# Optimization experiments

Hardware: AMD Instinct MI355X
Metric: run time of the kernel (lower is better)

## Reference

```python
import jax, jax.numpy as jnp
import numpy as np

COMMITMENT_COST = 0.25


def setup_inputs() -> dict:
    key = jax.random.key(0)
    k1, k2 = jax.random.split(key)
    inputs = jax.random.normal(k1, (32, 1024, 256), dtype=jnp.float32)
    codebook = jax.random.normal(k2, (8192, 256), dtype=jnp.float32)
    return {"inputs": inputs, "codebook": codebook}


def reference(inputs, codebook):
    input_shape = inputs.shape
    D = codebook.shape[1]
    K = codebook.shape[0]
    flat = inputs.reshape(-1, D)                      # [N, D]
    N = flat.shape[0]

    distances = (
        jnp.sum(flat * flat, axis=1, keepdims=True)
        + jnp.sum(codebook * codebook, axis=1)
        - 2.0 * flat @ codebook.T
    )                                                  # [N, K]
    idx = jnp.argmin(distances, axis=1)               # [N]

    # gather (equivalent to one-hot @ codebook)
    quantized = jnp.take(codebook, idx, axis=0).reshape(input_shape)

    # straight-through estimator
    quantized_st = inputs + jax.lax.stop_gradient(quantized - inputs)

    e_latent_loss = jnp.mean((jax.lax.stop_gradient(quantized_st) - inputs) ** 2)
    q_latent_loss = jnp.mean((quantized - jax.lax.stop_gradient(inputs)) ** 2)
    commitment_loss = COMMITMENT_COST * e_latent_loss
    codebook_loss = q_latent_loss
    vq_loss = commitment_loss + codebook_loss

    # perplexity of codebook usage (avg one-hot probs)
    counts = jnp.zeros((K,), dtype=inputs.dtype).at[idx].add(1.0)
    avg_probs = counts / N
    perplexity = jnp.exp(-jnp.sum(avg_probs * jnp.log(avg_probs + 1e-10)))

    tokens = idx.reshape(input_shape[:-1])
    return quantized_st, tokens, vq_loss, commitment_loss, codebook_loss, perplexity
```

## Files before the change

### kernel.cpp

```cpp
#include <hip/hip_runtime.h>
#include <stdint.h>

typedef unsigned short u16;
typedef unsigned long long u64;

#define N_ROWS 32768
#define DIM 256
#define K_CODES 8192
#define TAU 0.3f

#define A_OFF     0ull
#define B_OFF     16777216ull
#define CN_OFF    20971520ull
#define PART1_OFF 21004288ull
#define PART2_OFF 22052864ull
#define IDX_OFF   22577152ull
#define HIST_OFF  22708224ull
#define CNT_OFF   22740992ull
#define FLAG_OFF  22741008ull
#define LOSS_OFF  22872080ull
#define CBT_OFF   23068672ull
#define GMIN2_OFF 31457280ull

#define OUT_Q 0
#define OUT_T 8388608
#define OUT_S 8421376

#define BM 128
#define BN 128
#define BK 64
#define JSPLIT 4
#define NT (4 * ((K_CODES / JSPLIT) / BN))
#define RSPLIT 4

#define PACK_INF ((((u64)0xFF800000u) << 32) | 0xFFFFFFFFull)

typedef _Float16 half8 __attribute__((ext_vector_type(8)));
typedef float floatx4 __attribute__((ext_vector_type(4)));

__device__ __forceinline__ void gload_lds16(const void* g, void* l) {
    __builtin_amdgcn_global_load_lds(
        (const __attribute__((address_space(1))) void*)g,
        (__attribute__((address_space(3))) void*)l,
        16, 0, 0);
}

__device__ __forceinline__ unsigned sortable(float v) {
    unsigned u = __float_as_uint(v);
    return (u & 0x80000000u) ? ~u : (u | 0x80000000u);
}
__device__ __forceinline__ float unsortable(unsigned u) {
    return (u & 0x80000000u) ? __uint_as_float(u & 0x7fffffffu) : __uint_as_float(~u);
}
__device__ __forceinline__ u64 shfl64x(u64 v, int m) {
    return ((u64)(unsigned)__shfl_xor((int)(v >> 32), m, 64) << 32) |
           (unsigned)__shfl_xor((int)(v & 0xffffffffu), m, 64);
}
__device__ __forceinline__ u64 u64min(u64 a, u64 b) { return a < b ? a : b; }
__device__ __forceinline__ u64 u64max(u64 a, u64 b) { return a > b ? a : b; }

__global__ void prep(const float* __restrict__ inp, const float* __restrict__ cb,
                     u16* __restrict__ A, u16* __restrict__ B, float* __restrict__ cn,
                     unsigned int* __restrict__ hist, int* __restrict__ cnt) {
    if (blockIdx.x >= 5120) {
        int i = (blockIdx.x - 5120) * 256 + threadIdx.x;
        if (i < K_CODES) hist[i] = 0u;
        else if (i < K_CODES + 4) cnt[i - K_CODES] = 0;
        return;
    }
    int g = blockIdx.x * 256 + threadIdx.x;
    int row = g >> 5;
    int kc = (g & 31) << 3;
    bool isA = row < N_ROWS;
    const float* src = isA ? inp + (size_t)row * DIM + kc
                           : cb + (size_t)(row - N_ROWS) * DIM + kc;
    u16* dst = isA ? A + (size_t)row * DIM + kc
                   : B + (size_t)(row - N_ROWS) * DIM + kc;
    float4 x0 = *(const float4*)(src);
    float4 x1 = *(const float4*)(src + 4);
    float xs[8] = {x0.x, x0.y, x0.z, x0.w, x1.x, x1.y, x1.z, x1.w};
    half8 hv;
    float s = 0.f;
#pragma unroll
    for (int i = 0; i < 8; ++i) {
        hv[i] = (_Float16)xs[i];
        s = fmaf(xs[i], xs[i], s);
    }
    *(half8*)(dst) = hv;
    if (!isA) {
#pragma unroll
        for (int m = 1; m <= 16; m <<= 1) s += __shfl_xor(s, m, 64);
        if ((g & 31) == 0) cn[row - N_ROWS] = s;
    }
}

__global__ void transpose_cb(const float* __restrict__ cb, float* __restrict__ cbT) {
    __shared__ float tile[64][65];
    const int tid = threadIdx.x;
    const int tj = blockIdx.x * 64;
    const int td = blockIdx.y * 64;
    const int c = (tid & 15) * 4;
    const int r0 = tid >> 4;
#pragma unroll
    for (int p = 0; p < 4; ++p) {
        int r = p * 16 + r0;
        float4 v = *(const float4*)(cb + (size_t)(tj + r) * DIM + td + c);
        tile[r][c] = v.x; tile[r][c + 1] = v.y; tile[r][c + 2] = v.z; tile[r][c + 3] = v.w;
    }
    __syncthreads();
#pragma unroll
    for (int p = 0; p < 4; ++p) {
        int rr = p * 16 + r0;
        float4 w = {tile[c][rr], tile[c + 1][rr], tile[c + 2][rr], tile[c + 3][rr]};
        *(float4*)(cbT + (size_t)(td + rr) * K_CODES + tj + c) = w;
    }
}

#define STAGE_T(T, BUFI)                                                      \
    {                                                                         \
        const int jc_ = (T) >> 2;                                             \
        const int kk_ = ((T) & 3) * BK;                                       \
        const int colBase_ = jBase + jc_ * BN;                                \
        _Pragma("unroll")                                                     \
        for (int it_ = 0; it_ < 4; ++it_) {                                   \
            int r_ = it_ * 32 + str;                                          \
            int cdat_ = sk16 ^ (r_ & 7);                                      \
            int ch_ = it_ * 256 + tid;                                        \
            gload_lds16(A + (size_t)(rowBase + r_) * DIM + kk_ + cdat_ * 8,   \
                        (char*)lsA[BUFI] + ch_ * 16);                         \
            gload_lds16(B + (size_t)(colBase_ + r_) * DIM + kk_ + cdat_ * 8,  \
                        (char*)lsB[BUFI] + ch_ * 16);                         \
        }                                                                     \
    }

__launch_bounds__(256, 2)
__global__ void vq_pass1(const u16* __restrict__ A, const u16* __restrict__ B,
                         const float* __restrict__ cn,
                         u64* __restrict__ part1, float* __restrict__ part2) {
    __shared__ __align__(16) _Float16 lsA[2][BM * BK];
    __shared__ __align__(16) _Float16 lsB[2][BN * BK];
    __shared__ u64 t1buf[BM];
    __shared__ float t2buf[BM];

    const int tid = threadIdx.x;
    const int lane = tid & 63;
    const int w = tid >> 6;
    const int wm = w >> 1, wn = w & 1;
    const int l15 = lane & 15;
    const int quad = lane >> 4;
    const int xm = l15 & 7;
    const int rowBase = blockIdx.x * BM;
    const int jBase = blockIdx.y * (K_CODES / JSPLIT);

    float d1[16], d2[16];
    unsigned idxr[16];
#pragma unroll
    for (int i = 0; i < 16; ++i) {
        d1[i] = __builtin_inff(); d2[i] = __builtin_inff(); idxr[i] = 0xffffffffu;
    }

    const int str = tid >> 3;
    const int sk16 = tid & 7;

    STAGE_T(0, 0);
    asm volatile("s_waitcnt vmcnt(0)" ::: "memory");
    __builtin_amdgcn_s_barrier();
    asm volatile("" ::: "memory");

    floatx4 acc[4][4];
    int buf = 0;

#pragma unroll 1
    for (int t = 0; t < NT; ++t) {
        if (t + 1 < NT) STAGE_T(t + 1, buf ^ 1);

        if ((t & 3) == 0) {
#pragma unroll
            for (int mi = 0; mi < 4; ++mi)
#pragma unroll
                for (int ni = 0; ni < 4; ++ni)
                    acc[mi][ni] = (floatx4){0.f, 0.f, 0.f, 0.f};
        }

#pragma unroll
        for (int s = 0; s < 2; ++s) {
            const int koff = ((s * 4 + quad) ^ xm) * 8;
            half8 af[4], bf[4];
#pragma unroll
            for (int mi = 0; mi < 4; ++mi)
                af[mi] = *(const half8*)(lsA[buf] + (wm * 64 + mi * 16 + l15) * BK + koff);
#pragma unroll
            for (int ni = 0; ni < 4; ++ni)
                bf[ni] = *(const half8*)(lsB[buf] + (wn * 64 + ni * 16 + l15) * BK + koff);
#pragma unroll
            for (int mi = 0; mi < 4; ++mi)
#pragma unroll
                for (int ni = 0; ni < 4; ++ni)
                    acc[mi][ni] = __builtin_amdgcn_mfma_f32_16x16x32_f16(
                        af[mi], bf[ni], acc[mi][ni], 0, 0, 0);
        }

        if ((t & 3) == 3) {
            const int colBase = jBase + (t >> 2) * BN;
#pragma unroll
            for (int ni = 0; ni < 4; ++ni) {
                unsigned j = (unsigned)(colBase + wn * 64 + ni * 16 + l15);
                float cnj = cn[j];
#pragma unroll
                for (int mi = 0; mi < 4; ++mi) {
#pragma unroll
                    for (int r = 0; r < 4; ++r) {
                        int tr = mi * 4 + r;
                        float val = fmaf(-2.0f, acc[mi][ni][r], cnj);
                        bool lt = val < d1[tr];
                        float sec = lt ? d1[tr] : val;
                        d2[tr] = fminf(d2[tr], sec);
                        d1[tr] = lt ? val : d1[tr];
                        idxr[tr] = lt ? j : idxr[tr];
                    }
                }
            }
        }

        asm volatile("s_waitcnt vmcnt(0)" ::: "memory");
        __builtin_amdgcn_s_barrier();
        asm volatile("" ::: "memory");
        buf ^= 1;
    }

    u64 m1[16];
#pragma unroll
    for (int tr = 0; tr < 16; ++tr)
        m1[tr] = ((u64)sortable(d1[tr]) << 32) | idxr[tr];
#pragma unroll
    for (int m = 1; m <= 8; m <<= 1)
#pragma unroll
        for (int tr = 0; tr < 16; ++tr) {
            u64 o1 = shfl64x(m1[tr], m);
            float o2 = __shfl_xor(d2[tr], m, 64);
            u64 n1 = u64min(m1[tr], o1);
            float big = unsortable((unsigned)(u64max(m1[tr], o1) >> 32));
            d2[tr] = fminf(big, fminf(d2[tr], o2));
            m1[tr] = n1;
        }

    if (wn == 0 && l15 == 0) {
#pragma unroll
        for (int tr = 0; tr < 16; ++tr) {
            int rl = wm * 64 + (tr >> 2) * 16 + quad * 4 + (tr & 3);
            t1buf[rl] = m1[tr]; t2buf[rl] = d2[tr];
        }
    }
    __syncthreads();
    if (wn == 1 && l15 == 0) {
#pragma unroll
        for (int tr = 0; tr < 16; ++tr) {
            int rl = wm * 64 + (tr >> 2) * 16 + quad * 4 + (tr & 3);
            u64 o1 = t1buf[rl];
            float o2 = t2buf[rl];
            u64 n1 = u64min(m1[tr], o1);
            float big = unsortable((unsigned)(u64max(m1[tr], o1) >> 32));
            float n2 = fminf(big, fminf(d2[tr], o2));
            size_t p = (size_t)(rowBase + rl) * JSPLIT + blockIdx.y;
            part1[p] = n1;
            part2[p] = n2;
        }
    }
}

__global__ void vq_merge(const u64* __restrict__ part1, const float* __restrict__ part2,
                         unsigned* __restrict__ idx32,
                         int* __restrict__ flaglist, int* __restrict__ cnt,
                         u64* __restrict__ gmin2) {
    int row = blockIdx.x * 256 + threadIdx.x;
    u64 m1 = PACK_INF;
    float f2 = __builtin_inff();
#pragma unroll
    for (int y = 0; y < JSPLIT; ++y) {
        u64 p1 = part1[(size_t)row * JSPLIT + y];
        float p2 = part2[(size_t)row * JSPLIT + y];
        u64 n1 = u64min(m1, p1);
        float big = unsortable((unsigned)(u64max(m1, p1) >> 32));
        f2 = fminf(big, fminf(f2, p2));
        m1 = n1;
    }
    gmin2[row] = PACK_INF;
    idx32[row] = (unsigned)(m1 & 0xffffffffu);
    float f1 = unsortable((unsigned)(m1 >> 32));
    if (f2 - f1 < TAU) {
        int p = atomicAdd(cnt, 1);
        flaglist[p] = row;
    }
}

__global__ void vq_recompute(const float* __restrict__ inp, const float* __restrict__ cbT,
                             const float* __restrict__ cn, const int* __restrict__ flaglist,
                             const int* __restrict__ cnt, u64* __restrict__ gmin2) {
    __shared__ float xsT[DIM][8];
    __shared__ u64 wred[8][8];
    const int tid = threadIdx.x;
    const int w = tid >> 6, lane = tid & 63;
    const int n = *cnt;
    const int base = blockIdx.x * 8;
    if (base >= n) return;

    {
        int li = base + w;
        int row = flaglist[li < n ? li : (n - 1)];
        float4 a = ((const float4*)(inp + (size_t)row * DIM))[lane];
        int d0 = lane * 4;
        xsT[d0 + 0][w] = a.x; xsT[d0 + 1][w] = a.y;
        xsT[d0 + 2][w] = a.z; xsT[d0 + 3][w] = a.w;
    }
    __syncthreads();

    const int cbase = blockIdx.y * (K_CODES / RSPLIT) + tid * 4;
    float4 acc[8];
#pragma unroll
    for (int r = 0; r < 8; ++r) acc[r] = (float4){0.f, 0.f, 0.f, 0.f};

    float4 cv = *(const float4*)(cbT + cbase);
#pragma unroll 4
    for (int d = 0; d < DIM - 1; ++d) {
        float4 nx = *(const float4*)(cbT + (size_t)(d + 1) * K_CODES + cbase);
        float4 xa = *(const float4*)&xsT[d][0];
        float4 xb = *(const float4*)&xsT[d][4];
        float xv[8] = {xa.x, xa.y, xa.z, xa.w, xb.x, xb.y, xb.z, xb.w};
#pragma unroll
        for (int r = 0; r < 8; ++r) {
            acc[r].x = fmaf(xv[r], cv.x, acc[r].x);
            acc[r].y = fmaf(xv[r], cv.y, acc[r].y);
            acc[r].z = fmaf(xv[r], cv.z, acc[r].z);
            acc[r].w = fmaf(xv[r], cv.w, acc[r].w);
        }
        cv = nx;
    }
    {
        const int d = DIM - 1;
        float4 xa = *(const float4*)&xsT[d][0];
        float4 xb = *(const float4*)&xsT[d][4];
        float xv[8] = {xa.x, xa.y, xa.z, xa.w, xb.x, xb.y, xb.z, xb.w};
#pragma unroll
        for (int r = 0; r < 8; ++r) {
            acc[r].x = fmaf(xv[r], cv.x, acc[r].x);
            acc[r].y = fmaf(xv[r], cv.y, acc[r].y);
            acc[r].z = fmaf(xv[r], cv.z, acc[r].z);
            acc[r].w = fmaf(xv[r], cv.w, acc[r].w);
        }
    }

    u64 best[8];
    float4 cn4 = *(const float4*)(cn + cbase);
#pragma unroll
    for (int r = 0; r < 8; ++r) {
        float d0 = cn4.x - 2.0f * acc[r].x;
        float d1 = cn4.y - 2.0f * acc[r].y;
        float d2 = cn4.z - 2.0f * acc[r].z;
        float d3 = cn4.w - 2.0f * acc[r].w;
        u64 b = ((u64)sortable(d0) << 32) | (unsigned)(cbase + 0);
        b = u64min(b, ((u64)sortable(d1) << 32) | (unsigned)(cbase + 1));
        b = u64min(b, ((u64)sortable(d2) << 32) | (unsigned)(cbase + 2));
        b = u64min(b, ((u64)sortable(d3) << 32) | (unsigned)(cbase + 3));
        best[r] = b;
    }

#pragma unroll
    for (int m = 1; m <= 32; m <<= 1)
#pragma unroll
        for (int r = 0; r < 8; ++r) best[r] = u64min(best[r], shfl64x(best[r], m));
    if (lane < 8) wred[w][lane] = best[lane];
    __syncthreads();
    if (tid < 8 && base + tid < n) {
        u64 b = wred[0][tid];
#pragma unroll
        for (int ww = 1; ww < 8; ++ww) b = u64min(b, wred[ww][tid]);
        atomicMin(&gmin2[flaglist[base + tid]], b);
    }
}

__global__ void vq_writeback(const u64* __restrict__ gmin2, const int* __restrict__ flaglist,
                             const int* __restrict__ cnt, unsigned* __restrict__ idx32) {
    int i = blockIdx.x * 256 + threadIdx.x;
    if (i < *cnt) {
        int row = flaglist[i];
        idx32[row] = (unsigned)(gmin2[row] & 0xffffffffull);
    }
}

__global__ void vq_gather(const float* __restrict__ inp, const float* __restrict__ cb,
                          const unsigned* __restrict__ idx32, float* __restrict__ out,
                          float* __restrict__ losspart, unsigned int* __restrict__ hist) {
    __shared__ float red[4];
    int w = threadIdx.x >> 6, lane = threadIdx.x & 63;
    int i = blockIdx.x * 4 + w;
    unsigned idx = idx32[i];
    float4 c = ((const float4*)(cb + (size_t)idx * DIM))[lane];
    float4 x = ((const float4*)(inp + (size_t)i * DIM))[lane];
    ((float4*)(out + OUT_Q))[(size_t)i * 64 + lane] = c;
    float dx = c.x - x.x, dy = c.y - x.y, dz = c.z - x.z, dw = c.w - x.w;
    float s = dx * dx + dy * dy + dz * dz + dw * dw;
#pragma unroll
    for (int m = 32; m; m >>= 1) s += __shfl_xor(s, m, 64);
    if (lane == 0) {
        out[OUT_T + i] = (float)idx;
        red[w] = s;
        atomicAdd(&hist[idx], 1u);
    }
    __syncthreads();
    if (threadIdx.x == 0)
        losspart[blockIdx.x] = red[0] + red[1] + red[2] + red[3];
}

__global__ void vq_finalize(const unsigned int* __restrict__ hist,
                            const float* __restrict__ losspart, float* __restrict__ out) {
    __shared__ float redp[256], redl[256];
    int tid = threadIdx.x;
    float sp = 0.f, sl = 0.f;
    for (int k = tid; k < K_CODES; k += 256) {
        float p = (float)hist[k] * (1.0f / (float)N_ROWS);
        sp += p * logf(p + 1e-10f);
        sl += losspart[k];
    }
    redp[tid] = sp; redl[tid] = sl;
    __syncthreads();
    for (int st = 128; st; st >>= 1) {
        if (tid < st) { redp[tid] += redp[tid + st]; redl[tid] += redl[tid + st]; }
        __syncthreads();
    }
    if (tid == 0) {
        float perp = expf(-redp[0]);
        float e = redl[0] / 8388608.0f;
        out[OUT_S + 0] = 1.25f * e;
        out[OUT_S + 1] = 0.25f * e;
        out[OUT_S + 2] = e;
        out[OUT_S + 3] = perp;
    }
}

extern "C" void kernel_launch(void* const* d_in, const int* in_sizes, int n_in,
                              void* d_out, int out_size, void* d_ws, size_t ws_size,
                              hipStream_t stream) {
    const float* inp = (const float*)d_in[0];
    const float* cb = (const float*)d_in[1];
    float* out = (float*)d_out;
    char* ws = (char*)d_ws;
    u16* A = (u16*)(ws + A_OFF);
    u16* B = (u16*)(ws + B_OFF);
    float* cn = (float*)(ws + CN_OFF);
    u64* part1 = (u64*)(ws + PART1_OFF);
    float* part2 = (float*)(ws + PART2_OFF);
    unsigned* idx32 = (unsigned*)(ws + IDX_OFF);
    unsigned int* hist = (unsigned int*)(ws + HIST_OFF);
    int* cnt = (int*)(ws + CNT_OFF);
    int* flaglist = (int*)(ws + FLAG_OFF);
    float* losspart = (float*)(ws + LOSS_OFF);
    float* cbT = (float*)(ws + CBT_OFF);
    u64* gmin2 = (u64*)(ws + GMIN2_OFF);

    prep<<<5153, 256, 0, stream>>>(inp, cb, A, B, cn, hist, cnt);
    transpose_cb<<<dim3(K_CODES / 64, DIM / 64), 256, 0, stream>>>(cb, cbT);
    vq_pass1<<<dim3(N_ROWS / BM, JSPLIT), 256, 0, stream>>>(A, B, cn, part1, part2);
    vq_merge<<<N_ROWS / 256, 256, 0, stream>>>(part1, part2, idx32, flaglist, cnt, gmin2);
    vq_recompute<<<dim3(N_ROWS / 8, RSPLIT), 512, 0, stream>>>(inp, cbT, cn, flaglist, cnt, gmin2);
    vq_writeback<<<N_ROWS / 256, 256, 0, stream>>>(gmin2, flaglist, cnt, idx32);
    vq_gather<<<N_ROWS / 4, 256, 0, stream>>>(inp, cb, idx32, out, losspart, hist);
    vq_finalize<<<1, 256, 0, stream>>>(hist, losspart, out);
}
```

Before: 391.6 us.

## Fuse transpose into prep, drop writeback, split top-2 epilogue, persistent recompute grid

Folds the codebook transpose into the prep kernel and removes the separate writeback kernel, so vq_gather now reads gmin2 directly and overrides the index when a recomputed minimum exists. In pass1, JSPLIT drops from 4 to 2, and half of each tile's top-2 distance update is deferred into the next tile's iteration so it can overlap the next stage's loads. The top-2 update now uses fmed3 for the second-best value. vq_recompute becomes a grid-stride loop over a fixed 512-block grid instead of one block per 8 rows. These changes cut kernel launches and idle blocks, at the cost of lower pass1 grid parallelism and gmin2 reads for every row.

```diff
diff --git a/kernel.cpp b/kernel.cpp
--- a/kernel.cpp
+++ b/kernel.cpp
@@ -29,9 +29,10 @@
 #define BM 128
 #define BN 128
 #define BK 64
-#define JSPLIT 4
+#define JSPLIT 2
 #define NT (4 * ((K_CODES / JSPLIT) / BN))
 #define RSPLIT 4
+#define RGRID 512
 
 #define PACK_INF ((((u64)0xFF800000u) << 32) | 0xFFFFFFFFull)
 
@@ -61,14 +62,39 @@
 
 __global__ void prep(const float* __restrict__ inp, const float* __restrict__ cb,
                      u16* __restrict__ A, u16* __restrict__ B, float* __restrict__ cn,
-                     unsigned int* __restrict__ hist, int* __restrict__ cnt) {
+                     unsigned int* __restrict__ hist, int* __restrict__ cnt,
+                     float* __restrict__ cbT) {
+    __shared__ float tile[64][65];
+    const int tid = threadIdx.x;
+
+    if (blockIdx.x >= 5153) {
+        const int bx = blockIdx.x - 5153;
+        const int tj = (bx & 127) * 64;
+        const int td = (bx >> 7) * 64;
+        const int c = (tid & 15) * 4;
+        const int r0 = tid >> 4;
+#pragma unroll
+        for (int p = 0; p < 4; ++p) {
+            int r = p * 16 + r0;
+            float4 v = *(const float4*)(cb + (size_t)(tj + r) * DIM + td + c);
+            tile[r][c] = v.x; tile[r][c + 1] = v.y; tile[r][c + 2] = v.z; tile[r][c + 3] = v.w;
+        }
+        __syncthreads();
+#pragma unroll
+        for (int p = 0; p < 4; ++p) {
+            int rr = p * 16 + r0;
+            float4 w = {tile[c][rr], tile[c + 1][rr], tile[c + 2][rr], tile[c + 3][rr]};
+            *(float4*)(cbT + (size_t)(td + rr) * K_CODES + tj + c) = w;
+        }
+        return;
+    }
     if (blockIdx.x >= 5120) {
-        int i = (blockIdx.x - 5120) * 256 + threadIdx.x;
+        int i = (blockIdx.x - 5120) * 256 + tid;
         if (i < K_CODES) hist[i] = 0u;
         else if (i < K_CODES + 4) cnt[i - K_CODES] = 0;
         return;
     }
-    int g = blockIdx.x * 256 + threadIdx.x;
+    int g = blockIdx.x * 256 + tid;
     int row = g >> 5;
     int kc = (g & 31) << 3;
     bool isA = row < N_ROWS;
@@ -91,28 +117,6 @@
 #pragma unroll
         for (int m = 1; m <= 16; m <<= 1) s += __shfl_xor(s, m, 64);
         if ((g & 31) == 0) cn[row - N_ROWS] = s;
-    }
-}
-
-__global__ void transpose_cb(const float* __restrict__ cb, float* __restrict__ cbT) {
-    __shared__ float tile[64][65];
-    const int tid = threadIdx.x;
-    const int tj = blockIdx.x * 64;
-    const int td = blockIdx.y * 64;
-    const int c = (tid & 15) * 4;
-    const int r0 = tid >> 4;
-#pragma unroll
-    for (int p = 0; p < 4; ++p) {
-        int r = p * 16 + r0;
-        float4 v = *(const float4*)(cb + (size_t)(tj + r) * DIM + td + c);
-        tile[r][c] = v.x; tile[r][c + 1] = v.y; tile[r][c + 2] = v.z; tile[r][c + 3] = v.w;
-    }
-    __syncthreads();
-#pragma unroll
-    for (int p = 0; p < 4; ++p) {
-        int rr = p * 16 + r0;
-        float4 w = {tile[c][rr], tile[c + 1][rr], tile[c + 2][rr], tile[c + 3][rr]};
-        *(float4*)(cbT + (size_t)(td + rr) * K_CODES + tj + c) = w;
     }
 }
 
@@ -133,6 +137,25 @@
         }                                                                     \
     }
 
+#define TOP2NI(JC, NI)                                                        \
+    {                                                                         \
+        unsigned j_ = (unsigned)(jBase + (JC) * BN + wn * 64 + (NI) * 16 + l15); \
+        float cnj_ = cn[j_];                                                  \
+        _Pragma("unroll")                                                     \
+        for (int mi_ = 0; mi_ < 4; ++mi_) {                                   \
+            _Pragma("unroll")                                                 \
+            for (int r_ = 0; r_ < 4; ++r_) {                                  \
+                int tr_ = mi_ * 4 + r_;                                       \
+                float val_ = fmaf(-2.0f, acc[mi_][NI][r_], cnj_);             \
+                float nd2_ = __builtin_amdgcn_fmed3f(d1[tr_], d2[tr_], val_); \
+                bool lt_ = val_ < d1[tr_];                                    \
+                d1[tr_] = fminf(d1[tr_], val_);                               \
+                idxr[tr_] = lt_ ? j_ : idxr[tr_];                             \
+                d2[tr_] = nd2_;                                               \
+            }                                                                 \
+        }                                                                     \
+    }
+
 __launch_bounds__(256, 2)
 __global__ void vq_pass1(const u16* __restrict__ A, const u16* __restrict__ B,
                          const float* __restrict__ cn,
@@ -175,6 +198,10 @@
         if (t + 1 < NT) STAGE_T(t + 1, buf ^ 1);
 
         if ((t & 3) == 0) {
+            if (t >= 4) {
+                TOP2NI((t >> 2) - 1, 2);
+                TOP2NI((t >> 2) - 1, 3);
+            }
 #pragma unroll
             for (int mi = 0; mi < 4; ++mi)
 #pragma unroll
@@ -201,25 +228,8 @@
         }
 
         if ((t & 3) == 3) {
-            const int colBase = jBase + (t >> 2) * BN;
-#pragma unroll
-            for (int ni = 0; ni < 4; ++ni) {
-                unsigned j = (unsigned)(colBase + wn * 64 + ni * 16 + l15);
-                float cnj = cn[j];
-#pragma unroll
-                for (int mi = 0; mi < 4; ++mi) {
-#pragma unroll
-                    for (int r = 0; r < 4; ++r) {
-                        int tr = mi * 4 + r;
-                        float val = fmaf(-2.0f, acc[mi][ni][r], cnj);
-                        bool lt = val < d1[tr];
-                        float sec = lt ? d1[tr] : val;
-                        d2[tr] = fminf(d2[tr], sec);
-                        d1[tr] = lt ? val : d1[tr];
-                        idxr[tr] = lt ? j : idxr[tr];
-                    }
-                }
-            }
+            TOP2NI(t >> 2, 0);
+            TOP2NI(t >> 2, 1);
         }
 
         asm volatile("s_waitcnt vmcnt(0)" ::: "memory");
@@ -227,6 +237,8 @@
         asm volatile("" ::: "memory");
         buf ^= 1;
     }
+    TOP2NI((NT >> 2) - 1, 2);
+    TOP2NI((NT >> 2) - 1, 3);
 
     u64 m1[16];
 #pragma unroll
@@ -301,99 +313,94 @@
     const int tid = threadIdx.x;
     const int w = tid >> 6, lane = tid & 63;
     const int n = *cnt;
-    const int base = blockIdx.x * 8;
-    if (base >= n) return;
-
-    {
-        int li = base + w;
-        int row = flaglist[li < n ? li : (n - 1)];
-        float4 a = ((const float4*)(inp + (size_t)row * DIM))[lane];
-        int d0 = lane * 4;
-        xsT[d0 + 0][w] = a.x; xsT[d0 + 1][w] = a.y;
-        xsT[d0 + 2][w] = a.z; xsT[d0 + 3][w] = a.w;
-    }
-    __syncthreads();
-
     const int cbase = blockIdx.y * (K_CODES / RSPLIT) + tid * 4;
-    float4 acc[8];
-#pragma unroll
-    for (int r = 0; r < 8; ++r) acc[r] = (float4){0.f, 0.f, 0.f, 0.f};
-
-    float4 cv = *(const float4*)(cbT + cbase);
+
+#pragma unroll 1
+    for (int base = blockIdx.x * 8; base < n; base += RGRID * 8) {
+        {
+            int li = base + w;
+            int row = flaglist[li < n ? li : (n - 1)];
+            float4 a = ((const float4*)(inp + (size_t)row * DIM))[lane];
+            int d0 = lane * 4;
+            xsT[d0 + 0][w] = a.x; xsT[d0 + 1][w] = a.y;
+            xsT[d0 + 2][w] = a.z; xsT[d0 + 3][w] = a.w;
+        }
+        __syncthreads();
+
+        float4 acc[8];
+#pragma unroll
+        for (int r = 0; r < 8; ++r) acc[r] = (float4){0.f, 0.f, 0.f, 0.f};
+
+        float4 cv = *(const float4*)(cbT + cbase);
 #pragma unroll 4
-    for (int d = 0; d < DIM - 1; ++d) {
-        float4 nx = *(const float4*)(cbT + (size_t)(d + 1) * K_CODES + cbase);
-        float4 xa = *(const float4*)&xsT[d][0];
-        float4 xb = *(const float4*)&xsT[d][4];
-        float xv[8] = {xa.x, xa.y, xa.z, xa.w, xb.x, xb.y, xb.z, xb.w};
+        for (int d = 0; d < DIM - 1; ++d) {
+            float4 nx = *(const float4*)(cbT + (size_t)(d + 1) * K_CODES + cbase);
+            float4 xa = *(const float4*)&xsT[d][0];
+            float4 xb = *(const float4*)&xsT[d][4];
+            float xv[8] = {xa.x, xa.y, xa.z, xa.w, xb.x, xb.y, xb.z, xb.w};
+#pragma unroll
+            for (int r = 0; r < 8; ++r) {
+                acc[r].x = fmaf(xv[r], cv.x, acc[r].x);
+                acc[r].y = fmaf(xv[r], cv.y, acc[r].y);
+                acc[r].z = fmaf(xv[r], cv.z, acc[r].z);
+                acc[r].w = fmaf(xv[r], cv.w, acc[r].w);
+            }
+            cv = nx;
+        }
+        {
+            const int d = DIM - 1;
+            float4 xa = *(const float4*)&xsT[d][0];
+            float4 xb = *(const float4*)&xsT[d][4];
+            float xv[8] = {xa.x, xa.y, xa.z, xa.w, xb.x, xb.y, xb.z, xb.w};
+#pragma unroll
+            for (int r = 0; r < 8; ++r) {
+                acc[r].x = fmaf(xv[r], cv.x, acc[r].x);
+                acc[r].y = fmaf(xv[r], cv.y, acc[r].y);
+                acc[r].z = fmaf(xv[r], cv.z, acc[r].z);
+                acc[r].w = fmaf(xv[r], cv.w, acc[r].w);
+            }
+        }
+
+        u64 best[8];
+        float4 cn4 = *(const float4*)(cn + cbase);
 #pragma unroll
         for (int r = 0; r < 8; ++r) {
-            acc[r].x = fmaf(xv[r], cv.x, acc[r].x);
-            acc[r].y = fmaf(xv[r], cv.y, acc[r].y);
-            acc[r].z = fmaf(xv[r], cv.z, acc[r].z);
-            acc[r].w = fmaf(xv[r], cv.w, acc[r].w);
-        }
-        cv = nx;
-    }
-    {
-        const int d = DIM - 1;
-        float4 xa = *(const float4*)&xsT[d][0];
-        float4 xb = *(const float4*)&xsT[d][4];
-        float xv[8] = {xa.x, xa.y, xa.z, xa.w, xb.x, xb.y, xb.z, xb.w};
-#pragma unroll
-        for (int r = 0; r < 8; ++r) {
-            acc[r].x = fmaf(xv[r], cv.x, acc[r].x);
-            acc[r].y = fmaf(xv[r], cv.y, acc[r].y);
-            acc[r].z = fmaf(xv[r], cv.z, acc[r].z);
-            acc[r].w = fmaf(xv[r], cv.w, acc[r].w);
-        }
-    }
-
-    u64 best[8];
-    float4 cn4 = *(const float4*)(cn + cbase);
-#pragma unroll
-    for (int r = 0; r < 8; ++r) {
-        float d0 = cn4.x - 2.0f * acc[r].x;
-        float d1 = cn4.y - 2.0f * acc[r].y;
-        float d2 = cn4.z - 2.0f * acc[r].z;
-        float d3 = cn4.w - 2.0f * acc[r].w;
-        u64 b = ((u64)sortable(d0) << 32) | (unsigned)(cbase + 0);
-        b = u64min(b, ((u64)sortable(d1) << 32) | (unsigned)(cbase + 1));
-        b = u64min(b, ((u64)sortable(d2) << 32) | (unsigned)(cbase + 2));
-        b = u64min(b, ((u64)sortable(d3) << 32) | (unsigned)(cbase + 3));
-        best[r] = b;
-    }
-
-#pragma unroll
-    for (int m = 1; m <= 32; m <<= 1)
-#pragma unroll
-        for (int r = 0; r < 8; ++r) best[r] = u64min(best[r], shfl64x(best[r], m));
-    if (lane < 8) wred[w][lane] = best[lane];
-    __syncthreads();
-    if (tid < 8 && base + tid < n) {
-        u64 b = wred[0][tid];
-#pragma unroll
-        for (int ww = 1; ww < 8; ++ww) b = u64min(b, wred[ww][tid]);
-        atomicMin(&gmin2[flaglist[base + tid]], b);
-    }
-}
-
-__global__ void vq_writeback(const u64* __restrict__ gmin2, const int* __restrict__ flaglist,
-                             const int* __restrict__ cnt, unsigned* __restrict__ idx32) {
-    int i = blockIdx.x * 256 + threadIdx.x;
-    if (i < *cnt) {
-        int row = flaglist[i];
-        idx32[row] = (unsigned)(gmin2[row] & 0xffffffffull);
+            float e0 = cn4.x - 2.0f * acc[r].x;
+            float e1 = cn4.y - 2.0f * acc[r].y;
+            float e2 = cn4.z - 2.0f * acc[r].z;
+            float e3 = cn4.w - 2.0f * acc[r].w;
+            u64 b = ((u64)sortable(e0) << 32) | (unsigned)(cbase + 0);
+            b = u64min(b, ((u64)sortable(e1) << 32) | (unsigned)(cbase + 1));
+            b = u64min(b, ((u64)sortable(e2) << 32) | (unsigned)(cbase + 2));
+            b = u64min(b, ((u64)sortable(e3) << 32) | (unsigned)(cbase + 3));
+            best[r] = b;
+        }
+
+#pragma unroll
+        for (int m = 1; m <= 32; m <<= 1)
+#pragma unroll
+            for (int r = 0; r < 8; ++r) best[r] = u64min(best[r], shfl64x(best[r], m));
+        if (lane < 8) wred[w][lane] = best[lane];
+        __syncthreads();
+        if (tid < 8 && base + tid < n) {
+            u64 b = wred[0][tid];
+#pragma unroll
+            for (int ww = 1; ww < 8; ++ww) b = u64min(b, wred[ww][tid]);
+            atomicMin(&gmin2[flaglist[base + tid]], b);
+        }
     }
 }
 
 __global__ void vq_gather(const float* __restrict__ inp, const float* __restrict__ cb,
-                          const unsigned* __restrict__ idx32, float* __restrict__ out,
+                          const unsigned* __restrict__ idx32,
+                          const u64* __restrict__ gmin2, float* __restrict__ out,
                           float* __restrict__ losspart, unsigned int* __restrict__ hist) {
     __shared__ float red[4];
     int w = threadIdx.x >> 6, lane = threadIdx.x & 63;
     int i = blockIdx.x * 4 + w;
     unsigned idx = idx32[i];
+    u64 g = gmin2[i];
+    if (g != PACK_INF) idx = (unsigned)(g & 0xffffffffull);
     float4 c = ((const float4*)(cb + (size_t)idx * DIM))[lane];
     float4 x = ((const float4*)(inp + (size_t)i * DIM))[lane];
     ((float4*)(out + OUT_Q))[(size_t)i * 64 + lane] = c;
@@ -457,12 +464,10 @@
     float* cbT = (float*)(ws + CBT_OFF);
     u64* gmin2 = (u64*)(ws + GMIN2_OFF);
 
-    prep<<<5153, 256, 0, stream>>>(inp, cb, A, B, cn, hist, cnt);
-    transpose_cb<<<dim3(K_CODES / 64, DIM / 64), 256, 0, stream>>>(cb, cbT);
+    prep<<<5665, 256, 0, stream>>>(inp, cb, A, B, cn, hist, cnt, cbT);
     vq_pass1<<<dim3(N_ROWS / BM, JSPLIT), 256, 0, stream>>>(A, B, cn, part1, part2);
     vq_merge<<<N_ROWS / 256, 256, 0, stream>>>(part1, part2, idx32, flaglist, cnt, gmin2);
-    vq_recompute<<<dim3(N_ROWS / 8, RSPLIT), 512, 0, stream>>>(inp, cbT, cn, flaglist, cnt, gmin2);
-    vq_writeback<<<N_ROWS / 256, 256, 0, stream>>>(gmin2, flaglist, cnt, idx32);
-    vq_gather<<<N_ROWS / 4, 256, 0, stream>>>(inp, cb, idx32, out, losspart, hist);
+    vq_recompute<<<dim3(RGRID, RSPLIT), 512, 0, stream>>>(inp, cbT, cn, flaglist, cnt, gmin2);
+    vq_gather<<<N_ROWS / 4, 256, 0, stream>>>(inp, cb, idx32, gmin2, out, losspart, hist);
     vq_finalize<<<1, 256, 0, stream>>>(hist, losspart, out);
 }
```

Result: no change. 390.7 us (-0.2%).
